# Kernel optimization log

Measured on AMD Instinct MI355X. Metric: run time of the kernel, lower is better.

Reference implementation:

```python
import jax, jax.numpy as jnp
import numpy as np
from jax import lax

VOCAB, EMB, HID, TAGS = 8000, 300, 512, 24  # hidden_dim=512 -> 256 per direction
B, S = 128, 512
H2 = HID // 2


def setup_inputs() -> dict:
    key = jax.random.key(0)
    ks = jax.random.split(key, 16)
    sc = 0.05
    inp = {
        "chars": jax.random.randint(ks[0], (B, S), 0, VOCAB),
        "tags": jax.random.randint(ks[1], (B, S), 0, TAGS),
        "mask": jnp.ones((B, S), dtype=bool),
        "emb": jax.random.normal(ks[2], (VOCAB, EMB), jnp.float32) * sc,
        # PyTorch LSTM layout: gates stacked [i, f, g, o]
        "w_ih_f": jax.random.normal(ks[3], (4 * H2, EMB), jnp.float32) * sc,
        "w_hh_f": jax.random.normal(ks[4], (4 * H2, H2), jnp.float32) * sc,
        "b_f": jax.random.normal(ks[5], (4 * H2,), jnp.float32) * sc,  # b_ih + b_hh fused
        "w_ih_b": jax.random.normal(ks[6], (4 * H2, EMB), jnp.float32) * sc,
        "w_hh_b": jax.random.normal(ks[7], (4 * H2, H2), jnp.float32) * sc,
        "b_b": jax.random.normal(ks[8], (4 * H2,), jnp.float32) * sc,
        "w_out": jax.random.normal(ks[9], (TAGS, HID), jnp.float32) * sc,
        "b_out": jax.random.normal(ks[10], (TAGS,), jnp.float32) * sc,
        "trans": jax.random.normal(ks[11], (TAGS, TAGS), jnp.float32) * sc,
        "start_trans": jax.random.normal(ks[12], (TAGS,), jnp.float32) * sc,
        "end_trans": jax.random.normal(ks[13], (TAGS,), jnp.float32) * sc,
    }
    return inp


def _lstm_dir(x, w_ih, w_hh, b, reverse):
    # x: [B, S, E] -> h: [B, S, H2]
    gx = jnp.einsum('bse,ge->bsg', x, w_ih) + b  # [B, S, 4*H2]

    def step(carry, g_t):
        h, c = carry
        g = g_t + h @ w_hh.T
        i, f, gg, o = jnp.split(g, 4, axis=-1)
        c = jax.nn.sigmoid(f) * c + jax.nn.sigmoid(i) * jnp.tanh(gg)
        h = jax.nn.sigmoid(o) * jnp.tanh(c)
        return (h, c), h

    init = (jnp.zeros((x.shape[0], H2), x.dtype), jnp.zeros((x.shape[0], H2), x.dtype))
    _, hs = lax.scan(step, init, jnp.swapaxes(gx, 0, 1), reverse=reverse)
    return jnp.swapaxes(hs, 0, 1)


def _crf_loss(emissions, tags, mask, trans, start_trans, end_trans):
    # torchcrf log-likelihood, reduction='mean'; loss = -mean
    b, s, t = emissions.shape
    maskf = mask.astype(emissions.dtype)
    # numerator: score of gold path
    em_t = jnp.take_along_axis(emissions, tags[..., None], axis=2)[..., 0]  # [B,S]
    tr_t = trans[tags[:, :-1], tags[:, 1:]]  # [B,S-1]
    score = start_trans[tags[:, 0]] + em_t[:, 0]
    score = score + jnp.sum((em_t[:, 1:] + tr_t) * maskf[:, 1:], axis=1)
    seq_ends = jnp.sum(mask.astype(jnp.int32), axis=1) - 1  # [B]
    last_tags = jnp.take_along_axis(tags, seq_ends[:, None], axis=1)[:, 0]
    score = score + end_trans[last_tags]
    # denominator: forward algorithm via scan
    alpha0 = start_trans + emissions[:, 0]  # [B,T]

    def step(alpha, inputs):
        em, m = inputs  # em [B,T], m [B]
        nxt = jax.nn.logsumexp(alpha[:, :, None] + trans[None] + em[:, None, :], axis=1)
        alpha = jnp.where(m[:, None], nxt, alpha)
        return alpha, None

    alpha, _ = lax.scan(step, alpha0,
                        (jnp.swapaxes(emissions[:, 1:], 0, 1), jnp.swapaxes(mask[:, 1:], 0, 1)))
    log_z = jax.nn.logsumexp(alpha + end_trans, axis=1)  # [B]
    llh = score - log_z
    return -jnp.mean(llh)


def reference(chars, tags, mask, emb, w_ih_f, w_hh_f, b_f, w_ih_b, w_hh_b, b_b,
              w_out, b_out, trans, start_trans, end_trans):
    x = emb[chars]  # [B,S,E]
    h_f = _lstm_dir(x, w_ih_f, w_hh_f, b_f, reverse=False)
    h_b = _lstm_dir(x, w_ih_b, w_hh_b, b_b, reverse=True)
    lstm_out = jnp.concatenate([h_f, h_b], axis=-1)  # [B,S,HID]
    emissions = jnp.einsum('bsh,th->bst', lstm_out, w_out) + b_out  # [B,S,TAGS]
    return _crf_loss(emissions, tags, mask, trans, start_trans, end_trans)
```

## Files before the change

kernel.cpp:

```cpp
#include <hip/hip_runtime.h>
#include <math.h>

#define BB   128
#define SS   512
#define EMBD 300
#define VOC  8000
#define NTAG 24
#define BSD  (BB*SS)

#define SW   400.0f
#define SH   512.0f
#define INVQ (1.0f / (400.0f * 512.0f))

typedef unsigned int   u32;
typedef unsigned short u16;
typedef unsigned char  u8;

__device__ __forceinline__ int idot4(u32 a, u32 b, int c) {
#if __has_builtin(__builtin_amdgcn_sdot4)
    return __builtin_amdgcn_sdot4((int)a, (int)b, c, false);
#else
    int s = c;
    #pragma unroll
    for (int e = 0; e < 4; ++e) {
        int xa = ((int)(a << (24 - 8 * e))) >> 24;
        int xb = ((int)(b << (24 - 8 * e))) >> 24;
        s += xa * xb;
    }
    return s;
#endif
}
__device__ __forceinline__ u32 rdlane(u32 v, int l) {
#if __has_builtin(__builtin_amdgcn_readlane)
    return (u32)__builtin_amdgcn_readlane((int)v, l);
#else
    return (u32)__shfl((int)v, l);
#endif
}
__device__ __forceinline__ void bar_lds() {
    asm volatile("s_waitcnt lgkmcnt(0)" ::: "memory");
    __builtin_amdgcn_s_barrier();
}
__device__ __forceinline__ float sigm(float x) { return 1.0f / (1.0f + __expf(-x)); }
__device__ __forceinline__ float tanh_fast(float x) {
    return 1.0f - 2.0f / (__expf(2.0f * x) + 1.0f);
}
__device__ __forceinline__ int qclamp(float x, float s) {
    int v = (int)rintf(x * s);
    return v > 127 ? 127 : (v < -127 ? -127 : v);
}
__device__ __forceinline__ u32 q4(const float* p, float s) {
    u32 r = 0;
    #pragma unroll
    for (int e = 0; e < 4; ++e)
        r |= ((u32)(qclamp(p[e], s) & 0xFF)) << (8 * e);
    return r;
}

__global__ __launch_bounds__(512)
void k_packW(const float* __restrict__ w_hh_f, const float* __restrict__ w_hh_b,
             const float* __restrict__ w_out,
             u32* __restrict__ wreg, uint4* __restrict__ wlds,
             uint4* __restrict__ wstr, u32* __restrict__ woq)
{
    const int dir = blockIdx.x;
    const int t   = threadIdx.x;
    const float* w = dir ? w_hh_b : w_hh_f;
    const float* rowA = w + (size_t)t * 256;
    const float* rowB = w + (size_t)(t + 512) * 256;

    for (int q = 0; q < 16; ++q) {
        wreg[((size_t)(dir * 32 + q) * 512) + t]      = q4(rowA + 4 * q, SW);
        wreg[((size_t)(dir * 32 + 16 + q) * 512) + t] = q4(rowB + 4 * q, SW);
    }
    for (int qq = 0; qq < 7; ++qq) {
        uint4 va, vb;
        va.x = q4(rowA + 4 * (16 + 4 * qq + 0), SW);
        va.y = q4(rowA + 4 * (16 + 4 * qq + 1), SW);
        va.z = q4(rowA + 4 * (16 + 4 * qq + 2), SW);
        va.w = q4(rowA + 4 * (16 + 4 * qq + 3), SW);
        vb.x = q4(rowB + 4 * (16 + 4 * qq + 0), SW);
        vb.y = q4(rowB + 4 * (16 + 4 * qq + 1), SW);
        vb.z = q4(rowB + 4 * (16 + 4 * qq + 2), SW);
        vb.w = q4(rowB + 4 * (16 + 4 * qq + 3), SW);
        wlds[((size_t)(dir * 14 + qq) * 512) + t]     = va;
        wlds[((size_t)(dir * 14 + 7 + qq) * 512) + t] = vb;
    }
    for (int qq = 0; qq < 5; ++qq) {
        uint4 va, vb;
        va.x = q4(rowA + 4 * (44 + 4 * qq + 0), SW);
        va.y = q4(rowA + 4 * (44 + 4 * qq + 1), SW);
        va.z = q4(rowA + 4 * (44 + 4 * qq + 2), SW);
        va.w = q4(rowA + 4 * (44 + 4 * qq + 3), SW);
        vb.x = q4(rowB + 4 * (44 + 4 * qq + 0), SW);
        vb.y = q4(rowB + 4 * (44 + 4 * qq + 1), SW);
        vb.z = q4(rowB + 4 * (44 + 4 * qq + 2), SW);
        vb.w = q4(rowB + 4 * (44 + 4 * qq + 3), SW);
        wstr[((size_t)(dir * 10 + qq) * 512) + t]     = va;
        wstr[((size_t)(dir * 10 + 5 + qq) * 512) + t] = vb;
    }
    for (int i = t; i < NTAG * 64; i += 512) {
        const int tag = i >> 6, q = i & 63;
        woq[(size_t)dir * NTAG * 64 + i] =
            q4(w_out + (size_t)tag * 512 + dir * 256 + 4 * q, SW);
    }
}

__global__ __launch_bounds__(256)
void k_gxtab(const float* __restrict__ emb,
             const float* __restrict__ w_f, const float* __restrict__ bias_f,
             const float* __restrict__ w_b, const float* __restrict__ bias_b,
             u16* __restrict__ gxtab)
{
    const int dir = blockIdx.z;
    const float* W    = dir ? w_b    : w_f;
    const float* bias = dir ? bias_b : bias_f;
    u16* out = gxtab + (size_t)dir * VOC * 1024;
    const int r0 = blockIdx.y * 64;
    const int c0 = blockIdx.x * 128;

    __shared__ float As[16][65];
    __shared__ float Bs[16][129];

    const int tid = threadIdx.x;
    const int kk = tid & 15;
    const int rr = tid >> 4;
    const int ty = tid >> 4;
    const int tx = tid & 15;

    float acc[4][8] = {};

    for (int kt = 0; kt < EMBD; kt += 16) {
        const int k = kt + kk;
        const bool kok = (k < EMBD);
        #pragma unroll
        for (int p = 0; p < 4; ++p)
            As[kk][rr + p * 16] = kok ? emb[(size_t)(r0 + rr + p * 16) * EMBD + k] : 0.0f;
        #pragma unroll
        for (int p = 0; p < 8; ++p)
            Bs[kk][rr + p * 16] = kok ? W[(size_t)(c0 + rr + p * 16) * EMBD + k] : 0.0f;
        __syncthreads();
        #pragma unroll
        for (int q = 0; q < 16; ++q) {
            float av[4], bv[8];
            #pragma unroll
            for (int i = 0; i < 4; ++i) av[i] = As[q][ty * 4 + i];
            #pragma unroll
            for (int jj = 0; jj < 8; ++jj) bv[jj] = Bs[q][jj * 16 + tx];
            #pragma unroll
            for (int i = 0; i < 4; ++i)
                #pragma unroll
                for (int jj = 0; jj < 8; ++jj)
                    acc[i][jj] = fmaf(av[i], bv[jj], acc[i][jj]);
        }
        __syncthreads();
    }

    #pragma unroll
    for (int i = 0; i < 4; ++i) {
        const size_t rb = (size_t)(r0 + ty * 4 + i) * 1024;
        #pragma unroll
        for (int jj = 0; jj < 8; ++jj) {
            const int cl = c0 + jj * 16 + tx;
            out[rb + cl] = __builtin_bit_cast(u16, (_Float16)(acc[i][jj] + bias[cl]));
        }
    }
}

__global__ __launch_bounds__(512, 2)
void k_lstm_rl(const int* __restrict__ chars, const u16* __restrict__ gxtab,
               const u32* __restrict__ wreg, const uint4* __restrict__ wlds,
               const uint4* __restrict__ wstr,
               u32* __restrict__ hst)
{
    const int bid = blockIdx.x;
    const int dir = bid >> 7;
    const int b   = bid & 127;
    const int tid = threadIdx.x;

    __shared__ __align__(16) uint4 ldsW[14 * 512];
    __shared__ __align__(16) u32   hq[2][64];
    __shared__ __align__(16) float2 xg[256];
    __shared__ int chlds[SS];

    chlds[tid] = chars[(size_t)b * SS + tid];
    {
        const uint4* wl = wlds + (size_t)dir * 14 * 512;
        #pragma unroll
        for (int q = 0; q < 14; ++q) ldsW[q * 512 + tid] = wl[(size_t)q * 512 + tid];
    }

    u32 WR[32];
    {
        const u32* wrp = wreg + (size_t)dir * 32 * 512 + tid;
        #pragma unroll
        for (int q = 0; q < 32; ++q) WR[q] = wrp[(size_t)q * 512];
    }
    const uint4* wsp = wstr + (size_t)dir * 10 * 512 + tid;

    const u16* gxp = gxtab + (size_t)dir * VOC * 1024;

    float c = 0.0f;
    u32 hreg = 0u;
    __syncthreads();

    const int t0 = dir ? (SS - 1) : 0;
    u16 gA = gxp[(size_t)chlds[t0] * 1024 + tid];
    u16 gB = gxp[(size_t)chlds[t0] * 1024 + 512 + tid];

    int cur = 0;
    #pragma unroll 1
    for (int sloc = 0; sloc < SS; ++sloc) {
        const int t = dir ? (SS - 1 - sloc) : sloc;

        u16 gA_n = 0, gB_n = 0;
        if (sloc < SS - 1) {
            const int tn = dir ? (t - 1) : (t + 1);
            const size_t o = (size_t)chlds[tn] * 1024 + tid;
            gA_n = gxp[o];
            gB_n = gxp[o + 512];
        }
        uint4 s[10];
        #pragma unroll
        for (int qq = 0; qq < 10; ++qq) s[qq] = wsp[(size_t)qq * 512];

        int aA = 0, aB = 0;
        #pragma unroll
        for (int q = 0; q < 16; ++q) {
            const u32 hs = rdlane(hreg, q);
            aA = idot4(WR[q], hs, aA);
            aB = idot4(WR[16 + q], hs, aB);
        }
        #pragma unroll
        for (int qq = 0; qq < 7; ++qq) {
            const uint4 wa = ldsW[qq * 512 + tid];
            const uint4 wb = ldsW[(7 + qq) * 512 + tid];
            const u32 h0 = rdlane(hreg, 16 + 4 * qq + 0);
            const u32 h1 = rdlane(hreg, 16 + 4 * qq + 1);
            const u32 h2 = rdlane(hreg, 16 + 4 * qq + 2);
            const u32 h3 = rdlane(hreg, 16 + 4 * qq + 3);
            aA = idot4(wa.x, h0, aA); aB = idot4(wb.x, h0, aB);
            aA = idot4(wa.y, h1, aA); aB = idot4(wb.y, h1, aB);
            aA = idot4(wa.z, h2, aA); aB = idot4(wb.z, h2, aB);
            aA = idot4(wa.w, h3, aA); aB = idot4(wb.w, h3, aB);
        }
        #pragma unroll
        for (int qq = 0; qq < 5; ++qq) {
            const uint4 wa = s[qq];
            const uint4 wb = s[5 + qq];
            const u32 h0 = rdlane(hreg, 44 + 4 * qq + 0);
            const u32 h1 = rdlane(hreg, 44 + 4 * qq + 1);
            const u32 h2 = rdlane(hreg, 44 + 4 * qq + 2);
            const u32 h3 = rdlane(hreg, 44 + 4 * qq + 3);
            aA = idot4(wa.x, h0, aA); aB = idot4(wb.x, h0, aB);
            aA = idot4(wa.y, h1, aA); aB = idot4(wb.y, h1, aB);
            aA = idot4(wa.z, h2, aA); aB = idot4(wb.z, h2, aB);
            aA = idot4(wa.w, h3, aA); aB = idot4(wb.w, h3, aB);
        }
        const float apreA = (float)aA * INVQ + (float)__builtin_bit_cast(_Float16, gA);
        const float apreB = (float)aB * INVQ + (float)__builtin_bit_cast(_Float16, gB);

        if (tid >= 256) xg[tid - 256] = make_float2(sigm(apreA), sigm(apreB));
        bar_lds();

        if (tid < 256) {
            const float2 fo = xg[tid];
            const float ig = sigm(apreA);
            const float gg = tanh_fast(apreB);
            c = fmaf(fo.x, c, ig * gg);
            const float h = fo.y * tanh_fast(c);
            const int hi = qclamp(h, SH);
            ((u8*)hq[cur ^ 1])[tid] = (u8)(hi & 0xFF);
        }
        bar_lds();

        hreg = hq[cur ^ 1][tid & 63];
        if (tid < 64)
            hst[(((size_t)b * SS + t) * 2 + dir) * 64 + tid] = hreg;

        gA = gA_n; gB = gB_n;
        cur ^= 1;
    }
}

__global__ __launch_bounds__(256)
void k_emis(const u32* __restrict__ hst, const u32* __restrict__ woq,
            const float* __restrict__ b_out, float* __restrict__ emis)
{
    const int r0  = blockIdx.x * 32;
    const int tid = threadIdx.x;

    __shared__ __align__(16) u32 hs[32 * 132];
    __shared__ __align__(16) u32 wo[NTAG * 132];

    #pragma unroll
    for (int p = 0; p < 16; ++p) {
        const int idx = p * 256 + tid;
        const int row = idx >> 7, rest = idx & 127;
        hs[row * 132 + rest] = hst[((size_t)(r0 + row)) * 128 + rest];
    }
    for (int i = tid; i < NTAG * 128; i += 256) {
        const int tag = i >> 7, q = i & 127;
        const u32 v = (q < 64) ? woq[tag * 64 + q]
                               : woq[NTAG * 64 + tag * 64 + (q - 64)];
        wo[tag * 132 + q] = v;
    }
    __syncthreads();

    #pragma unroll
    for (int rep = 0; rep < 3; ++rep) {
        const int out = rep * 256 + tid;
        const int row = out / 24;
        const int tag = out - row * 24;
        const uint4* h4 = (const uint4*)&hs[row * 132];
        const uint4* w4 = (const uint4*)&wo[tag * 132];
        int e = 0;
        #pragma unroll
        for (int q = 0; q < 32; ++q) {
            const uint4 hv = h4[q];
            const uint4 wv = w4[q];
            e = idot4(wv.x, hv.x, e);
            e = idot4(wv.y, hv.y, e);
            e = idot4(wv.z, hv.z, e);
            e = idot4(wv.w, hv.w, e);
        }
        emis[(size_t)(r0 + row) * NTAG + tag] = (float)e * INVQ + b_out[tag];
    }
}

__global__ __launch_bounds__(64)
void k_crf(const float* __restrict__ emis, const int* __restrict__ tags,
           const float* __restrict__ trans, const float* __restrict__ start_tr,
           const float* __restrict__ end_tr, float* __restrict__ llh)
{
    const int b    = blockIdx.x;
    const int lane = threadIdx.x;
    const float* em = emis + (size_t)b * SS * NTAG;
    const int*   tg = tags + (size_t)b * SS;
    const bool active = (lane < NTAG);

    float trans_reg[NTAG];
    #pragma unroll
    for (int i = 0; i < NTAG; ++i)
        trans_reg[i] = active ? trans[i * NTAG + lane] : 0.0f;

    float sc = 0.0f;
    for (int t = lane; t < SS; t += 64) {
        const int tt = tg[t];
        sc += em[t * NTAG + tt];
        if (t > 0) sc += trans[tg[t - 1] * NTAG + tt];
    }
    #pragma unroll
    for (int off = 32; off > 0; off >>= 1) sc += __shfl_down(sc, off);

    float alpha = active ? (start_tr[lane] + em[lane]) : -1e30f;
    for (int t = 1; t < SS; ++t) {
        float v[NTAG];
        #pragma unroll
        for (int i = 0; i < NTAG; ++i)
            v[i] = __shfl(alpha, i) + trans_reg[i];
        float m = v[0];
        #pragma unroll
        for (int i = 1; i < NTAG; ++i) m = fmaxf(m, v[i]);
        float ssum = 0.0f;
        #pragma unroll
        for (int i = 0; i < NTAG; ++i) ssum += __expf(v[i] - m);
        const float e = active ? em[t * NTAG + lane] : 0.0f;
        alpha = active ? (m + __logf(ssum) + e) : -1e30f;
    }

    float v = alpha + (active ? end_tr[lane] : 0.0f);
    float m = v;
    #pragma unroll
    for (int off = 32; off > 0; off >>= 1) m = fmaxf(m, __shfl_down(m, off));
    m = __shfl(m, 0);
    float e = __expf(v - m);
    #pragma unroll
    for (int off = 32; off > 0; off >>= 1) e += __shfl_down(e, off);

    if (lane == 0) {
        const float logz  = m + __logf(e);
        const float score = sc + start_tr[tg[0]] + end_tr[tg[SS - 1]];
        llh[b] = score - logz;
    }
}

__global__ __launch_bounds__(64)
void k_final(const float* __restrict__ llh, float* __restrict__ out)
{
    const int lane = threadIdx.x;
    float v = llh[lane] + llh[lane + 64];
    #pragma unroll
    for (int off = 32; off > 0; off >>= 1) v += __shfl_down(v, off);
    if (lane == 0) out[0] = -(v * (1.0f / 128.0f));
}

extern "C" void kernel_launch(void* const* d_in, const int* in_sizes, int n_in,
                              void* d_out, int out_size, void* d_ws, size_t ws_size,
                              hipStream_t stream)
{
    (void)in_sizes; (void)n_in; (void)out_size; (void)ws_size;

    const int*   chars   = (const int*)d_in[0];
    const int*   tags    = (const int*)d_in[1];
    const float* emb     = (const float*)d_in[3];
    const float* w_ih_f  = (const float*)d_in[4];
    const float* w_hh_f  = (const float*)d_in[5];
    const float* b_f     = (const float*)d_in[6];
    const float* w_ih_b  = (const float*)d_in[7];
    const float* w_hh_b  = (const float*)d_in[8];
    const float* b_b     = (const float*)d_in[9];
    const float* w_out   = (const float*)d_in[10];
    const float* b_out   = (const float*)d_in[11];
    const float* trans   = (const float*)d_in[12];
    const float* start_t = (const float*)d_in[13];
    const float* end_t   = (const float*)d_in[14];

    char* ws = (char*)d_ws;
    size_t off = 0;
    auto carve = [&](size_t bytes) -> char* {
        char* p = ws + off;
        off += (bytes + 255) & ~(size_t)255;
        return p;
    };
    u16*   gxtab  = (u16*)carve((size_t)2 * VOC * 1024 * 2);
    u32*   wreg   = (u32*)carve((size_t)2 * 32 * 512 * 4);
    uint4* wlds   = (uint4*)carve((size_t)2 * 14 * 512 * 16);
    uint4* wstr   = (uint4*)carve((size_t)2 * 10 * 512 * 16);
    u32*   woq    = (u32*)carve((size_t)2 * NTAG * 64 * 4);
    u32*   hst    = (u32*)carve((size_t)BSD * 2 * 64 * 4);
    float* emis   = (float*)carve((size_t)BSD * NTAG * 4);
    float* llh    = (float*)carve(128 * 4);

    hipLaunchKernelGGL(k_packW, dim3(2), dim3(512), 0, stream,
                       w_hh_f, w_hh_b, w_out, wreg, wlds, wstr, woq);
    hipLaunchKernelGGL(k_gxtab, dim3(8, 125, 2), dim3(256), 0, stream,
                       emb, w_ih_f, b_f, w_ih_b, b_b, gxtab);
    hipLaunchKernelGGL(k_lstm_rl, dim3(256), dim3(512), 0, stream,
                       chars, gxtab, wreg, wlds, wstr, hst);
    hipLaunchKernelGGL(k_emis, dim3(BSD / 32), dim3(256), 0, stream,
                       hst, woq, b_out, emis);
    hipLaunchKernelGGL(k_crf, dim3(128), dim3(64), 0, stream,
                       emis, tags, trans, start_t, end_t, llh);
    hipLaunchKernelGGL(k_final, dim3(1), dim3(64), 0, stream,
                       llh, (float*)d_out);
}
```

Baseline: 1.107 ms.

## Quantize input projection table GEMM to int8 dot4 and retune LSTM step

Adds a pre-pass that quantizes the embedding table and input weights to int8, so the vocab-by-gates gx table is built with sdot4 integer dot products on packed data and vectorized loads, replacing the fp32 FMA GEMM. In the recurrent kernel it also makes the per-thread streamed weight layout contiguous, removes the branch around the next-step prefetch, and splits the dot-product accumulators into two chains to shorten dependency latency. It adds an extra pack kernel and more quantization error in the input projection.

```diff
diff --git a/kernel.cpp b/kernel.cpp
--- a/kernel.cpp
+++ b/kernel.cpp
@@ -12,6 +12,10 @@
 #define SH   512.0f
 #define INVQ (1.0f / (400.0f * 512.0f))
 
+#define SQE  440.0f
+#define INVQE (1.0f / (440.0f * 440.0f))
+#define KQ   80
+
 typedef unsigned int   u32;
 typedef unsigned short u16;
 typedef unsigned char  u8;
@@ -55,6 +59,30 @@
     for (int e = 0; e < 4; ++e)
         r |= ((u32)(qclamp(p[e], s) & 0xFF)) << (8 * e);
     return r;
+}
+__device__ __forceinline__ u32 q4g(const float* p, int n, float s) {
+    u32 r = 0;
+    #pragma unroll
+    for (int e = 0; e < 4; ++e) {
+        const int v = (e < n) ? qclamp(p[e], s) : 0;
+        r |= ((u32)(v & 0xFF)) << (8 * e);
+    }
+    return r;
+}
+
+__global__ __launch_bounds__(128)
+void k_packE(const float* __restrict__ emb, const float* __restrict__ w_ih_f,
+             const float* __restrict__ w_ih_b, u32* __restrict__ eq)
+{
+    const int row = blockIdx.x;
+    const int g   = threadIdx.x;
+    if (g >= KQ) return;
+    const float* src = (row < 8000) ? (emb + (size_t)row * EMBD)
+                     : (row < 9024) ? (w_ih_f + (size_t)(row - 8000) * EMBD)
+                                    : (w_ih_b + (size_t)(row - 9024) * EMBD);
+    const int ks = g * 4;
+    const int n  = (ks >= EMBD) ? 0 : ((EMBD - ks) >= 4 ? 4 : (EMBD - ks));
+    eq[(size_t)row * KQ + g] = (n == 4) ? q4(src + ks, SQE) : q4g(src + ks, n, SQE);
 }
 
 __global__ __launch_bounds__(512)
@@ -96,8 +124,8 @@
         vb.y = q4(rowB + 4 * (44 + 4 * qq + 1), SW);
         vb.z = q4(rowB + 4 * (44 + 4 * qq + 2), SW);
         vb.w = q4(rowB + 4 * (44 + 4 * qq + 3), SW);
-        wstr[((size_t)(dir * 10 + qq) * 512) + t]     = va;
-        wstr[((size_t)(dir * 10 + 5 + qq) * 512) + t] = vb;
+        wstr[((size_t)(dir * 512 + t)) * 10 + qq]     = va;
+        wstr[((size_t)(dir * 512 + t)) * 10 + 5 + qq] = vb;
     }
     for (int i = t; i < NTAG * 64; i += 512) {
         const int tag = i >> 6, q = i & 63;
@@ -107,42 +135,51 @@
 }
 
 __global__ __launch_bounds__(256)
-void k_gxtab(const float* __restrict__ emb,
-             const float* __restrict__ w_f, const float* __restrict__ bias_f,
-             const float* __restrict__ w_b, const float* __restrict__ bias_b,
+void k_gxtab(const u32* __restrict__ eq,
+             const float* __restrict__ bias_f, const float* __restrict__ bias_b,
              u16* __restrict__ gxtab)
 {
     const int dir = blockIdx.z;
-    const float* W    = dir ? w_b    : w_f;
     const float* bias = dir ? bias_b : bias_f;
     u16* out = gxtab + (size_t)dir * VOC * 1024;
     const int r0 = blockIdx.y * 64;
     const int c0 = blockIdx.x * 128;
 
-    __shared__ float As[16][65];
-    __shared__ float Bs[16][129];
+    const u32* A = eq + (size_t)r0 * KQ;
+    const u32* B = eq + (size_t)(8000 + dir * 1024 + c0) * KQ;
+
+    __shared__ u32 As[16][66];
+    __shared__ u32 Bs[16][130];
 
     const int tid = threadIdx.x;
-    const int kk = tid & 15;
-    const int rr = tid >> 4;
     const int ty = tid >> 4;
     const int tx = tid & 15;
 
-    float acc[4][8] = {};
-
-    for (int kt = 0; kt < EMBD; kt += 16) {
-        const int k = kt + kk;
-        const bool kok = (k < EMBD);
-        #pragma unroll
-        for (int p = 0; p < 4; ++p)
-            As[kk][rr + p * 16] = kok ? emb[(size_t)(r0 + rr + p * 16) * EMBD + k] : 0.0f;
-        #pragma unroll
-        for (int p = 0; p < 8; ++p)
-            Bs[kk][rr + p * 16] = kok ? W[(size_t)(c0 + rr + p * 16) * EMBD + k] : 0.0f;
+    int acc[4][8] = {};
+
+    for (int kt = 0; kt < 5; ++kt) {
+        {
+            const int r = tid >> 2, qd = tid & 3;
+            const uint4 v = *(const uint4*)&A[(size_t)r * KQ + kt * 16 + qd * 4];
+            As[qd * 4 + 0][r] = v.x;
+            As[qd * 4 + 1][r] = v.y;
+            As[qd * 4 + 2][r] = v.z;
+            As[qd * 4 + 3][r] = v.w;
+        }
+        #pragma unroll
+        for (int e = 0; e < 2; ++e) {
+            const int idx = tid * 2 + e;
+            const int r = idx >> 2, qd = idx & 3;
+            const uint4 v = *(const uint4*)&B[(size_t)r * KQ + kt * 16 + qd * 4];
+            Bs[qd * 4 + 0][r] = v.x;
+            Bs[qd * 4 + 1][r] = v.y;
+            Bs[qd * 4 + 2][r] = v.z;
+            Bs[qd * 4 + 3][r] = v.w;
+        }
         __syncthreads();
         #pragma unroll
         for (int q = 0; q < 16; ++q) {
-            float av[4], bv[8];
+            u32 av[4], bv[8];
             #pragma unroll
             for (int i = 0; i < 4; ++i) av[i] = As[q][ty * 4 + i];
             #pragma unroll
@@ -151,7 +188,7 @@
             for (int i = 0; i < 4; ++i)
                 #pragma unroll
                 for (int jj = 0; jj < 8; ++jj)
-                    acc[i][jj] = fmaf(av[i], bv[jj], acc[i][jj]);
+                    acc[i][jj] = idot4(av[i], bv[jj], acc[i][jj]);
         }
         __syncthreads();
     }
@@ -162,7 +199,8 @@
         #pragma unroll
         for (int jj = 0; jj < 8; ++jj) {
             const int cl = c0 + jj * 16 + tx;
-            out[rb + cl] = __builtin_bit_cast(u16, (_Float16)(acc[i][jj] + bias[cl]));
+            const float v = (float)acc[i][jj] * INVQE + bias[cl];
+            out[rb + cl] = __builtin_bit_cast(u16, (_Float16)v);
         }
     }
 }
@@ -196,7 +234,7 @@
         #pragma unroll
         for (int q = 0; q < 32; ++q) WR[q] = wrp[(size_t)q * 512];
     }
-    const uint4* wsp = wstr + (size_t)dir * 10 * 512 + tid;
+    const uint4* wsp = wstr + ((size_t)dir * 512 + tid) * 10;
 
     const u16* gxp = gxtab + (size_t)dir * VOC * 1024;
 
@@ -213,23 +251,24 @@
     for (int sloc = 0; sloc < SS; ++sloc) {
         const int t = dir ? (SS - 1 - sloc) : sloc;
 
-        u16 gA_n = 0, gB_n = 0;
-        if (sloc < SS - 1) {
-            const int tn = dir ? (t - 1) : (t + 1);
-            const size_t o = (size_t)chlds[tn] * 1024 + tid;
-            gA_n = gxp[o];
-            gB_n = gxp[o + 512];
-        }
+        const int tn = dir ? max(t - 1, 0) : min(t + 1, SS - 1);
+        const size_t po = (size_t)chlds[tn] * 1024 + tid;
+        const u16 gA_n = gxp[po];
+        const u16 gB_n = gxp[po + 512];
+
         uint4 s[10];
         #pragma unroll
-        for (int qq = 0; qq < 10; ++qq) s[qq] = wsp[(size_t)qq * 512];
-
-        int aA = 0, aB = 0;
-        #pragma unroll
-        for (int q = 0; q < 16; ++q) {
-            const u32 hs = rdlane(hreg, q);
-            aA = idot4(WR[q], hs, aA);
-            aB = idot4(WR[16 + q], hs, aB);
+        for (int qq = 0; qq < 10; ++qq) s[qq] = wsp[qq];
+
+        int aA0 = 0, aA1 = 0, aB0 = 0, aB1 = 0;
+        #pragma unroll
+        for (int q = 0; q < 16; q += 2) {
+            const u32 h0 = rdlane(hreg, q);
+            const u32 h1 = rdlane(hreg, q + 1);
+            aA0 = idot4(WR[q], h0, aA0);
+            aB0 = idot4(WR[16 + q], h0, aB0);
+            aA1 = idot4(WR[q + 1], h1, aA1);
+            aB1 = idot4(WR[16 + q + 1], h1, aB1);
         }
         #pragma unroll
         for (int qq = 0; qq < 7; ++qq) {
@@ -239,10 +278,10 @@
             const u32 h1 = rdlane(hreg, 16 + 4 * qq + 1);
             const u32 h2 = rdlane(hreg, 16 + 4 * qq + 2);
             const u32 h3 = rdlane(hreg, 16 + 4 * qq + 3);
-            aA = idot4(wa.x, h0, aA); aB = idot4(wb.x, h0, aB);
-            aA = idot4(wa.y, h1, aA); aB = idot4(wb.y, h1, aB);
-            aA = idot4(wa.z, h2, aA); aB = idot4(wb.z, h2, aB);
-            aA = idot4(wa.w, h3, aA); aB = idot4(wb.w, h3, aB);
+            aA0 = idot4(wa.x, h0, aA0); aB0 = idot4(wb.x, h0, aB0);
+            aA1 = idot4(wa.y, h1, aA1); aB1 = idot4(wb.y, h1, aB1);
+            aA0 = idot4(wa.z, h2, aA0); aB0 = idot4(wb.z, h2, aB0);
+            aA1 = idot4(wa.w, h3, aA1); aB1 = idot4(wb.w, h3, aB1);
         }
         #pragma unroll
         for (int qq = 0; qq < 5; ++qq) {
@@ -252,13 +291,15 @@
             const u32 h1 = rdlane(hreg, 44 + 4 * qq + 1);
             const u32 h2 = rdlane(hreg, 44 + 4 * qq + 2);
             const u32 h3 = rdlane(hreg, 44 + 4 * qq + 3);
-            aA = idot4(wa.x, h0, aA); aB = idot4(wb.x, h0, aB);
-            aA = idot4(wa.y, h1, aA); aB = idot4(wb.y, h1, aB);
-            aA = idot4(wa.z, h2, aA); aB = idot4(wb.z, h2, aB);
-            aA = idot4(wa.w, h3, aA); aB = idot4(wb.w, h3, aB);
-        }
-        const float apreA = (float)aA * INVQ + (float)__builtin_bit_cast(_Float16, gA);
-        const float apreB = (float)aB * INVQ + (float)__builtin_bit_cast(_Float16, gB);
+            aA0 = idot4(wa.x, h0, aA0); aB0 = idot4(wb.x, h0, aB0);
+            aA1 = idot4(wa.y, h1, aA1); aB1 = idot4(wb.y, h1, aB1);
+            aA0 = idot4(wa.z, h2, aA0); aB0 = idot4(wb.z, h2, aB0);
+            aA1 = idot4(wa.w, h3, aA1); aB1 = idot4(wb.w, h3, aB1);
+        }
+        const float apreA = (float)(aA0 + aA1) * INVQ
+                          + (float)__builtin_bit_cast(_Float16, gA);
+        const float apreB = (float)(aB0 + aB1) * INVQ
+                          + (float)__builtin_bit_cast(_Float16, gB);
 
         if (tid >= 256) xg[tid - 256] = make_float2(sigm(apreA), sigm(apreB));
         bar_lds();
@@ -269,8 +310,7 @@
             const float gg = tanh_fast(apreB);
             c = fmaf(fo.x, c, ig * gg);
             const float h = fo.y * tanh_fast(c);
-            const int hi = qclamp(h, SH);
-            ((u8*)hq[cur ^ 1])[tid] = (u8)(hi & 0xFF);
+            ((u8*)hq[cur ^ 1])[tid] = (u8)(qclamp(h, SH) & 0xFF);
         }
         bar_lds();
 
@@ -424,18 +464,21 @@
         return p;
     };
     u16*   gxtab  = (u16*)carve((size_t)2 * VOC * 1024 * 2);
+    u32*   eq     = (u32*)carve((size_t)10048 * KQ * 4);
     u32*   wreg   = (u32*)carve((size_t)2 * 32 * 512 * 4);
     uint4* wlds   = (uint4*)carve((size_t)2 * 14 * 512 * 16);
-    uint4* wstr   = (uint4*)carve((size_t)2 * 10 * 512 * 16);
+    uint4* wstr   = (uint4*)carve((size_t)2 * 512 * 10 * 16);
     u32*   woq    = (u32*)carve((size_t)2 * NTAG * 64 * 4);
     u32*   hst    = (u32*)carve((size_t)BSD * 2 * 64 * 4);
     float* emis   = (float*)carve((size_t)BSD * NTAG * 4);
     float* llh    = (float*)carve(128 * 4);
 
+    hipLaunchKernelGGL(k_packE, dim3(10048), dim3(128), 0, stream,
+                       emb, w_ih_f, w_ih_b, eq);
     hipLaunchKernelGGL(k_packW, dim3(2), dim3(512), 0, stream,
                        w_hh_f, w_hh_b, w_out, wreg, wlds, wstr, woq);
     hipLaunchKernelGGL(k_gxtab, dim3(8, 125, 2), dim3(256), 0, stream,
-                       emb, w_ih_f, b_f, w_ih_b, b_b, gxtab);
+                       eq, b_f, b_b, gxtab);
     hipLaunchKernelGGL(k_lstm_rl, dim3(256), dim3(512), 0, stream,
                        chars, gxtab, wreg, wlds, wstr, hst);
     hipLaunchKernelGGL(k_emis, dim3(BSD / 32), dim3(256), 0, stream,
```

Measured after the change: 1.002 ms. 9.5% less time.
